# Performance work log

Hardware: AMD Instinct MI355X
Metric: run time of the kernel (lower is better)

## Reference

```python
import jax, jax.numpy as jnp
import numpy as np
from jax import lax

Q = 3          # Self-ONN polynomial order
EPS = 1e-5     # InstanceNorm1d eps


def setup_inputs() -> dict:
    key = jax.random.key(0)
    k1, k2, k3 = jax.random.split(key, 3)
    B, Cin, L = 16, 128, 8192
    Cout, K = 128, 3
    x = jax.random.normal(k1, (B, Cin, L), dtype=jnp.float32)
    # Conv1d weight over power-expanded channels: [Cout, Cin*Q, K]
    W = jax.random.normal(k2, (Cout, Cin * Q, K), dtype=jnp.float32) * 0.05
    b = jax.random.normal(k3, (Cout,), dtype=jnp.float32) * 0.05
    return {"x": x, "W": W, "b": b}


def reference(x, W, b):
    x = jnp.repeat(x, 2, axis=-1)
    # Self-ONN power expansion: concat x^1..x^Q along channel dim -> (B, C*Q, 2L)
    powers = jnp.concatenate([x ** (i + 1) for i in range(Q)], axis=1)
    # Conv1d, stride 1, padding 1 (same length)
    out = lax.conv_general_dilated(
        powers, W,
        window_strides=(1,),
        padding=[(1, 1)],
        dimension_numbers=("NCH", "OIH", "NCH"),
    ) + b[None, :, None]
    # InstanceNorm1d (affine=False): normalize over length per (batch, channel)
    mean = jnp.mean(out, axis=-1, keepdims=True)
    var = jnp.var(out, axis=-1, keepdims=True)
    out = (out - mean) * lax.rsqrt(var + EPS)
    # Tanh activation (self.relu is nn.Tanh()); dropout=False -> no-op
    return jnp.tanh(out)
```

## Files before the change

kernel.cpp:

```cpp
#include <hip/hip_runtime.h>
#include <hip/hip_fp16.h>
#include <math.h>

#define BATCH 16
#define CIN   128
#define LIN   8192
#define COUT  128
#define LOUT  16384
#define KEXP  768
#define NT    128
#define NTILES (LIN/NT)
#define PCOLS 130
#define PCPAD 136
#define PSZ   (PCOLS*PCPAD)

typedef _Float16 f16x8 __attribute__((ext_vector_type(8)));
typedef float    f32x4 __attribute__((ext_vector_type(4)));

__global__ void prep_weights(const float* __restrict__ W,
                             _Float16* __restrict__ WE,
                             _Float16* __restrict__ WO) {
  int idx = blockIdx.x * 256 + threadIdx.x;
  int co = idx / KEXP;
  int k  = idx % KEXP;
  int sh = (k >= 384) ? 1 : 0;
  int cq = k - 384 * sh;
  const float* w = W + ((size_t)co * 384 + cq) * 3;
  float we, wo;
  if (sh == 0) { we = w[0];        wo = w[0] + w[1]; }
  else         { we = w[1] + w[2]; wo = w[2];        }
  int q  = cq >> 7;
  int c  = cq & 127;
  int ks = q * 8 + sh * 4 + (c >> 5);
  int kk = c & 31, quad = kk >> 3, j = kk & 7;
  int mtile = co >> 4, l15 = co & 15;
  size_t off = ((size_t)((mtile * 24 + ks) * 64) + quad * 16 + l15) * 8 + j;
  WE[off] = (_Float16)we;
  WO[off] = (_Float16)wo;
}


#define BUILD_PLANE(POW, P) do {                                           \
  _Pragma("unroll")                                                        \
  for (int slot = 0; slot < 5; ++slot) {                                   \
    if (slot < 4 || tail) {                                                \
      f16x8 w;                                                             \
      _Pragma("unroll")                                                    \
      for (int j = 0; j < 8; ++j) {                                        \
        float v = xv[slot][j];                                             \
        float pv = ((POW) == 1) ? v : (((POW) == 2) ? v * v : v * (v * v));\
        w[j] = (_Float16)pv;                                               \
      }                                                                    \
      *(f16x8*)((P) + woff[slot]) = w;                                     \
    }                                                                      \
  }                                                                        \
} while (0)

#define AFLOAD(DST, KS) do {                                               \
  _Pragma("unroll")                                                        \
  for (int fm = 0; fm < 4; ++fm) {                                         \
    int mt = wm * 4 + fm;                                                  \
    DST[fm] = *(const f16x8*)(Wsel + ((size_t)((mt * 24 + (KS)) * 64) + lane) * 8); \
  }                                                                        \
} while (0)

#define BFLOAD(DST, CUR, S) do {                                           \
  _Pragma("unroll")                                                        \
  for (int fn = 0; fn < 4; ++fn) {                                         \
    int colB = wn * 64 + fn * 16 + l15 + (((S) >> 2) + isO);               \
    DST[fn] = *(const f16x8*)((CUR) + colB * PCPAD + ((S) & 3) * 32 + kl); \
  }                                                                        \
} while (0)

__launch_bounds__(512, 2)
__global__ void conv_gemm(const float* __restrict__ x,
                          const _Float16* __restrict__ WE,
                          const _Float16* __restrict__ WO,
                          float* __restrict__ out,
                          float* __restrict__ stats) {
  extern __shared__ char smem[];
  float*    sstats = (float*)smem;
  _Float16* planes = (_Float16*)(smem + 1024);

  const int tile = blockIdx.x;
  const int b    = blockIdx.y;
  const int i0   = tile * NT;
  const int t    = threadIdx.x;
  const int lane = t & 63;
  const int wave = t >> 6;
  const int p    = wave >> 1;
  const int isO  = wave & 1;
  const int wm   = p >> 1, wn = p & 1;
  const int l15  = lane & 15, quad = lane >> 4;
  const int kl   = quad * 8;

  if (t < 128) { sstats[2 * t] = 0.f; sstats[2 * t + 1] = 0.f; }

  const float* xb = x + (size_t)b * CIN * LIN;
  const _Float16* Wsel = isO ? WO : WE;

  float xv[5][8];
  int   woff[5];
  const bool tail = (t < PCOLS * 16 - 2048);
#pragma unroll
  for (int slot = 0; slot < 5; ++slot) {
    const bool tval = (slot < 4) || tail;
    int task = t + 512 * slot;
    int g    = task / PCOLS;
    if (!tval) g = 0;
    int col  = task - g * PCOLS;
    int gi   = i0 - 1 + col;
    woff[slot] = col * PCPAD + g * 8;
    const bool ok = tval && gi >= 0 && gi < LIN;
    const float* px = xb + (size_t)g * 8 * LIN + gi;
#pragma unroll
    for (int j = 0; j < 8; ++j) {
      float v = 0.f;
      if (ok) v = px[(size_t)j * LIN];
      xv[slot][j] = v;
    }
  }

  f32x4 acc[4][4];
  const f32x4 zero = {0.f, 0.f, 0.f, 0.f};
#pragma unroll
  for (int fm = 0; fm < 4; ++fm)
#pragma unroll
    for (int fn = 0; fn < 4; ++fn) acc[fm][fn] = zero;

  f16x8 af[3][4], bf[2][4];
  AFLOAD(af[0], 0);
  AFLOAD(af[1], 1);
  BUILD_PLANE(1, planes);
  __syncthreads();

#pragma unroll
  for (int q = 0; q < 3; ++q) {
    _Float16* cur = planes + (size_t)(q & 1) * PSZ;
    BFLOAD(bf[0], cur, 0);
    if (q == 0)      BUILD_PLANE(2, planes + PSZ);
    else if (q == 1) BUILD_PLANE(3, planes);

#pragma unroll
    for (int s = 0; s < 8; ++s) {
      const int ks = q * 8 + s;
      if (ks + 2 < 24) AFLOAD(af[(ks + 2) % 3], ks + 2);
      if (s < 7)       BFLOAD(bf[(s + 1) & 1], cur, s + 1);
      __builtin_amdgcn_s_setprio(1);
#pragma unroll
      for (int fm = 0; fm < 4; ++fm)
#pragma unroll
        for (int fn = 0; fn < 4; ++fn)
          acc[fm][fn] = __builtin_amdgcn_mfma_f32_16x16x32_f16(af[ks % 3][fm], bf[s & 1][fn], acc[fm][fn], 0, 0, 0);
      __builtin_amdgcn_s_setprio(0);
    }
    __syncthreads();
  }

  float* orow_base = out + (size_t)b * COUT * LOUT + isO;
#pragma unroll
  for (int fm = 0; fm < 4; ++fm) {
#pragma unroll
    for (int r = 0; r < 4; ++r) {
      float s1 = 0.f, s2 = 0.f;
#pragma unroll
      for (int fn = 0; fn < 4; ++fn) {
        float v = acc[fm][fn][r];
        s1 += v;
        s2 += v * v;
      }
#pragma unroll
      for (int off = 8; off >= 1; off >>= 1) {
        s1 += __shfl_xor(s1, off, 64);
        s2 += __shfl_xor(s2, off, 64);
      }
      int co = wm * 64 + fm * 16 + quad * 4 + r;
      if (l15 == 0) {
        atomicAdd(&sstats[2 * co], s1);
        atomicAdd(&sstats[2 * co + 1], s2);
      }
      float* orow = orow_base + (size_t)co * LOUT;
#pragma unroll
      for (int fn = 0; fn < 4; ++fn) {
        int n = i0 + wn * 64 + fn * 16 + l15;
        orow[2 * n] = acc[fm][fn][r];
      }
    }
  }
  __syncthreads();
  if (t < 128) {
    atomicAdd(&stats[((size_t)b * COUT + t) * 2],     sstats[2 * t]);
    atomicAdd(&stats[((size_t)b * COUT + t) * 2 + 1], sstats[2 * t + 1]);
  }
}

__device__ inline float tanh_fast(float z) {
  float e = __expf(2.f * z);
  return 1.f - 2.f * __builtin_amdgcn_rcpf(e + 1.f);
}

__global__ void norm_tanh(float* __restrict__ out, const float* __restrict__ stats) {
  int row = blockIdx.x;
  float s1 = stats[2 * row], s2 = stats[2 * row + 1];
  const float invN = 1.f / (float)LOUT;
  float mean = s1 * invN;
  float var  = fmaxf(s2 * invN - mean * mean, 0.f);
  float inv  = rsqrtf(var + 1e-5f);
  float c0   = -mean * inv;
  float4* p = (float4*)(out + (size_t)row * LOUT);
  for (int i = threadIdx.x; i < LOUT / 4; i += 256) {
    float4 v = p[i];
    v.x = tanh_fast(fmaf(v.x, inv, c0));
    v.y = tanh_fast(fmaf(v.y, inv, c0));
    v.z = tanh_fast(fmaf(v.z, inv, c0));
    v.w = tanh_fast(fmaf(v.w, inv, c0));
    p[i] = v;
  }
}

extern "C" void kernel_launch(void* const* d_in, const int* in_sizes, int n_in,
                              void* d_out, int out_size, void* d_ws, size_t ws_size,
                              hipStream_t stream) {
  const float* x = (const float*)d_in[0];
  const float* W = (const float*)d_in[1];
  float* out = (float*)d_out;

  float*    stats = (float*)d_ws;
  _Float16* WE    = (_Float16*)((char*)d_ws + 16384);
  _Float16* WO    = WE + (size_t)COUT * KEXP;

  hipMemsetAsync(d_ws, 0, 16384, stream);
  prep_weights<<<dim3((COUT * KEXP) / 256), dim3(256), 0, stream>>>(W, WE, WO);

  size_t shmem = 1024 + (size_t)PSZ * 2 * 2;
  hipFuncSetAttribute(reinterpret_cast<const void*>(conv_gemm),
                      hipFuncAttributeMaxDynamicSharedMemorySize, (int)shmem);
  conv_gemm<<<dim3(NTILES, BATCH), dim3(512), shmem, stream>>>(x, WE, WO, out, stats);

  norm_tanh<<<dim3(BATCH * COUT), dim3(256), 0, stream>>>(out, stats);
}
```

Measured before the change: 276.5 us.

## Persistent conv GEMM with prefetched x tiles, fp16 powers and fp16 intermediate

The conv GEMM becomes persistent: 256 blocks each process four (batch, tile) work items, and the next item's x columns are gathered while the current item's MFMAs run. The x^2 and x^3 planes are now built in fp16 from the x plane in LDS instead of from fp32 registers. Stats go straight to global atomics without the per-block LDS reduction. When the workspace is large enough, the pre-normalisation output is stored as fp16 and read back by norm_tanh, halving that round trip, at the cost of precision before normalisation.

```diff
diff --git a/kernel.cpp b/kernel.cpp
--- a/kernel.cpp
+++ b/kernel.cpp
@@ -13,6 +13,7 @@
 #define PCOLS 130
 #define PCPAD 136
 #define PSZ   (PCOLS*PCPAD)
+#define NITEMS 4
 
 typedef _Float16 f16x8 __attribute__((ext_vector_type(8)));
 typedef float    f32x4 __attribute__((ext_vector_type(4)));
@@ -40,87 +41,107 @@
 }
 
 
-#define BUILD_PLANE(POW, P) do {                                           \
+#define AFLOAD(DST, KS) do {                                               \
+  _Pragma("unroll")                                                        \
+  for (int fm = 0; fm < 4; ++fm) {                                         \
+    int mt = wm * 4 + fm;                                                  \
+    DST[fm] = *(const f16x8*)(Wsel + ((size_t)((mt * 24 + (KS)) * 64) + lane) * 8); \
+  }                                                                        \
+} while (0)
+
+#define BFLOAD(DST, P, S) do {                                             \
+  const _Float16* pb = (P) + (((S) & 3) * 32) + kl;                        \
+  const int shft = (((S) >> 2) + isO);                                     \
+  _Pragma("unroll")                                                        \
+  for (int fn = 0; fn < 4; ++fn) {                                         \
+    int colB = wn * 64 + fn * 16 + l15 + shft;                             \
+    DST[fn] = *(const f16x8*)(pb + colB * PCPAD);                          \
+  }                                                                        \
+} while (0)
+
+#define BUILD_SQ(SRC, DST) do {                                            \
+  _Pragma("unroll")                                                        \
+  for (int slot = 0; slot < 5; ++slot) {                                   \
+    if (slot < 4 || tail) {                                                \
+      f16x8 v = *(f16x8*)((SRC) + woffv[slot]);                            \
+      *(f16x8*)((DST) + woffv[slot]) = v * v;                              \
+    }                                                                      \
+  }                                                                        \
+} while (0)
+
+#define BUILD_CU(P1P, P2P) do {                                            \
+  _Pragma("unroll")                                                        \
+  for (int slot = 0; slot < 5; ++slot) {                                   \
+    if (slot < 4 || tail) {                                                \
+      f16x8 v1 = *(f16x8*)((P1P) + woffv[slot]);                           \
+      f16x8 v2 = *(f16x8*)((P2P) + woffv[slot]);                           \
+      *(f16x8*)((P1P) + woffv[slot]) = v1 * v2;                            \
+    }                                                                      \
+  }                                                                        \
+} while (0)
+
+#define XGATHER(WI) do {                                                   \
+  const float* xbn = x + (size_t)((WI) >> 6) * CIN * LIN;                  \
+  const int i0n = ((WI) & 63) * NT;                                        \
+  _Pragma("unroll")                                                        \
+  for (int slot = 0; slot < 5; ++slot) {                                   \
+    const bool tval = (slot < 4) || tail;                                  \
+    int gi = i0n - 1 + colv[slot];                                         \
+    const bool ok = tval && gi >= 0 && gi < LIN;                           \
+    const float* px = xbn + (size_t)gv[slot] * 8 * LIN + gi;               \
+    _Pragma("unroll")                                                      \
+    for (int j = 0; j < 8; ++j) xn[slot][j] = ok ? px[(size_t)j * LIN] : 0.f; \
+  }                                                                        \
+} while (0)
+
+#define XWRITE(DST) do {                                                   \
   _Pragma("unroll")                                                        \
   for (int slot = 0; slot < 5; ++slot) {                                   \
     if (slot < 4 || tail) {                                                \
       f16x8 w;                                                             \
       _Pragma("unroll")                                                    \
-      for (int j = 0; j < 8; ++j) {                                        \
-        float v = xv[slot][j];                                             \
-        float pv = ((POW) == 1) ? v : (((POW) == 2) ? v * v : v * (v * v));\
-        w[j] = (_Float16)pv;                                               \
-      }                                                                    \
-      *(f16x8*)((P) + woff[slot]) = w;                                     \
+      for (int j = 0; j < 8; ++j) w[j] = (_Float16)xn[slot][j];            \
+      *(f16x8*)((DST) + woffv[slot]) = w;                                  \
     }                                                                      \
   }                                                                        \
 } while (0)
 
-#define AFLOAD(DST, KS) do {                                               \
-  _Pragma("unroll")                                                        \
-  for (int fm = 0; fm < 4; ++fm) {                                         \
-    int mt = wm * 4 + fm;                                                  \
-    DST[fm] = *(const f16x8*)(Wsel + ((size_t)((mt * 24 + (KS)) * 64) + lane) * 8); \
-  }                                                                        \
-} while (0)
-
-#define BFLOAD(DST, CUR, S) do {                                           \
-  _Pragma("unroll")                                                        \
-  for (int fn = 0; fn < 4; ++fn) {                                         \
-    int colB = wn * 64 + fn * 16 + l15 + (((S) >> 2) + isO);               \
-    DST[fn] = *(const f16x8*)((CUR) + colB * PCPAD + ((S) & 3) * 32 + kl); \
-  }                                                                        \
-} while (0)
-
+template<int F16OUT>
 __launch_bounds__(512, 2)
 __global__ void conv_gemm(const float* __restrict__ x,
                           const _Float16* __restrict__ WE,
                           const _Float16* __restrict__ WO,
                           float* __restrict__ out,
+                          _Float16* __restrict__ out16,
                           float* __restrict__ stats) {
   extern __shared__ char smem[];
-  float*    sstats = (float*)smem;
-  _Float16* planes = (_Float16*)(smem + 1024);
-
-  const int tile = blockIdx.x;
-  const int b    = blockIdx.y;
-  const int i0   = tile * NT;
+  _Float16* planes = (_Float16*)smem;
+
+  const int bid  = blockIdx.x;
   const int t    = threadIdx.x;
   const int lane = t & 63;
   const int wave = t >> 6;
-  const int p    = wave >> 1;
   const int isO  = wave & 1;
-  const int wm   = p >> 1, wn = p & 1;
+  const int wn   = (wave >> 1) & 1;
+  const int wm   = wave >> 2;
   const int l15  = lane & 15, quad = lane >> 4;
   const int kl   = quad * 8;
 
-  if (t < 128) { sstats[2 * t] = 0.f; sstats[2 * t + 1] = 0.f; }
-
-  const float* xb = x + (size_t)b * CIN * LIN;
   const _Float16* Wsel = isO ? WO : WE;
 
-  float xv[5][8];
-  int   woff[5];
   const bool tail = (t < PCOLS * 16 - 2048);
+  int colv[5], gv[5], woffv[5];
 #pragma unroll
   for (int slot = 0; slot < 5; ++slot) {
-    const bool tval = (slot < 4) || tail;
     int task = t + 512 * slot;
     int g    = task / PCOLS;
-    if (!tval) g = 0;
     int col  = task - g * PCOLS;
-    int gi   = i0 - 1 + col;
-    woff[slot] = col * PCPAD + g * 8;
-    const bool ok = tval && gi >= 0 && gi < LIN;
-    const float* px = xb + (size_t)g * 8 * LIN + gi;
-#pragma unroll
-    for (int j = 0; j < 8; ++j) {
-      float v = 0.f;
-      if (ok) v = px[(size_t)j * LIN];
-      xv[slot][j] = v;
-    }
+    colv[slot]  = col;
+    gv[slot]    = g;
+    woffv[slot] = col * PCPAD + g * 8;
   }
 
+  float xn[5][8];
   f32x4 acc[4][4];
   const f32x4 zero = {0.f, 0.f, 0.f, 0.f};
 #pragma unroll
@@ -131,66 +152,90 @@
   f16x8 af[3][4], bf[2][4];
   AFLOAD(af[0], 0);
   AFLOAD(af[1], 1);
-  BUILD_PLANE(1, planes);
+
+  XGATHER(bid);
+  XWRITE(planes);
   __syncthreads();
-
-#pragma unroll
-  for (int q = 0; q < 3; ++q) {
-    _Float16* cur = planes + (size_t)(q & 1) * PSZ;
-    BFLOAD(bf[0], cur, 0);
-    if (q == 0)      BUILD_PLANE(2, planes + PSZ);
-    else if (q == 1) BUILD_PLANE(3, planes);
-
-#pragma unroll
-    for (int s = 0; s < 8; ++s) {
-      const int ks = q * 8 + s;
-      if (ks + 2 < 24) AFLOAD(af[(ks + 2) % 3], ks + 2);
-      if (s < 7)       BFLOAD(bf[(s + 1) & 1], cur, s + 1);
-      __builtin_amdgcn_s_setprio(1);
-#pragma unroll
-      for (int fm = 0; fm < 4; ++fm)
-#pragma unroll
-        for (int fn = 0; fn < 4; ++fn)
-          acc[fm][fn] = __builtin_amdgcn_mfma_f32_16x16x32_f16(af[ks % 3][fm], bf[s & 1][fn], acc[fm][fn], 0, 0, 0);
-      __builtin_amdgcn_s_setprio(0);
+  BFLOAD(bf[0], planes, 0);
+
+  for (int item = 0; item < NITEMS; ++item) {
+    _Float16* cur = planes + (size_t)(item & 1) * PSZ;
+    _Float16* oth = planes + (size_t)((item & 1) ^ 1) * PSZ;
+    const int wiN = bid + 256 * (item + 1);
+    const bool more = (item < NITEMS - 1);
+
+#pragma unroll
+    for (int q = 0; q < 3; ++q) {
+      const _Float16* pq = (q == 1) ? oth : cur;
+#pragma unroll
+      for (int s = 0; s < 8; ++s) {
+        const int ks = q * 8 + s;
+        AFLOAD(af[(ks + 2) % 3], (ks + 2) % 24);
+        if (s < 7) BFLOAD(bf[(s + 1) & 1], pq, s + 1);
+        if (q == 0 && s == 0) BUILD_SQ(cur, oth);
+        if (q == 1 && s == 0) BUILD_CU(cur, oth);
+        if (q == 1 && s == 4) { if (more) XGATHER(wiN); }
+        if (q == 2 && s == 4) { if (more) XWRITE(oth); }
+        __builtin_amdgcn_s_setprio(1);
+#pragma unroll
+        for (int fm = 0; fm < 4; ++fm)
+#pragma unroll
+          for (int fn = 0; fn < 4; ++fn)
+            acc[fm][fn] = __builtin_amdgcn_mfma_f32_16x16x32_f16(af[ks % 3][fm], bf[s & 1][fn], acc[fm][fn], 0, 0, 0);
+        __builtin_amdgcn_s_setprio(0);
+      }
+      __syncthreads();
+      if (q == 0)      BFLOAD(bf[0], oth, 0);
+      else if (q == 1) BFLOAD(bf[0], cur, 0);
+      else if (more)   BFLOAD(bf[0], oth, 0);
     }
-    __syncthreads();
-  }
-
-  float* orow_base = out + (size_t)b * COUT * LOUT + isO;
-#pragma unroll
-  for (int fm = 0; fm < 4; ++fm) {
-#pragma unroll
-    for (int r = 0; r < 4; ++r) {
-      float s1 = 0.f, s2 = 0.f;
-#pragma unroll
-      for (int fn = 0; fn < 4; ++fn) {
-        float v = acc[fm][fn][r];
-        s1 += v;
-        s2 += v * v;
-      }
-#pragma unroll
-      for (int off = 8; off >= 1; off >>= 1) {
-        s1 += __shfl_xor(s1, off, 64);
-        s2 += __shfl_xor(s2, off, 64);
-      }
-      int co = wm * 64 + fm * 16 + quad * 4 + r;
-      if (l15 == 0) {
-        atomicAdd(&sstats[2 * co], s1);
-        atomicAdd(&sstats[2 * co + 1], s2);
-      }
-      float* orow = orow_base + (size_t)co * LOUT;
-#pragma unroll
-      for (int fn = 0; fn < 4; ++fn) {
-        int n = i0 + wn * 64 + fn * 16 + l15;
-        orow[2 * n] = acc[fm][fn][r];
+
+    const int wi = bid + 256 * item;
+    const int b  = wi >> 6;
+    const int i0 = (wi & 63) * NT;
+#pragma unroll
+    for (int fm = 0; fm < 4; ++fm) {
+#pragma unroll
+      for (int r = 0; r < 4; ++r) {
+        float s1 = 0.f, s2 = 0.f;
+#pragma unroll
+        for (int fn = 0; fn < 4; ++fn) {
+          float v = acc[fm][fn][r];
+          s1 += v;
+          s2 += v * v;
+        }
+#pragma unroll
+        for (int off = 8; off >= 1; off >>= 1) {
+          s1 += __shfl_xor(s1, off, 64);
+          s2 += __shfl_xor(s2, off, 64);
+        }
+        int co = wm * 64 + fm * 16 + quad * 4 + r;
+        if (l15 == 0) {
+          atomicAdd(&stats[((size_t)b * COUT + co) * 2],     s1);
+          atomicAdd(&stats[((size_t)b * COUT + co) * 2 + 1], s2);
+        }
+        if (F16OUT) {
+          _Float16* orow = out16 + ((size_t)b * COUT + co) * LOUT + isO;
+#pragma unroll
+          for (int fn = 0; fn < 4; ++fn) {
+            int n = i0 + wn * 64 + fn * 16 + l15;
+            orow[2 * n] = (_Float16)acc[fm][fn][r];
+          }
+        } else {
+          float* orow = out + ((size_t)b * COUT + co) * LOUT + isO;
+#pragma unroll
+          for (int fn = 0; fn < 4; ++fn) {
+            int n = i0 + wn * 64 + fn * 16 + l15;
+            orow[2 * n] = acc[fm][fn][r];
+          }
+        }
+        acc[fm][r < 4 ? 0 : 0][0] = acc[fm][0][0];
       }
     }
-  }
-  __syncthreads();
-  if (t < 128) {
-    atomicAdd(&stats[((size_t)b * COUT + t) * 2],     sstats[2 * t]);
-    atomicAdd(&stats[((size_t)b * COUT + t) * 2 + 1], sstats[2 * t + 1]);
+#pragma unroll
+    for (int fm = 0; fm < 4; ++fm)
+#pragma unroll
+      for (int fn = 0; fn < 4; ++fn) acc[fm][fn] = zero;
   }
 }
 
@@ -199,7 +244,9 @@
   return 1.f - 2.f * __builtin_amdgcn_rcpf(e + 1.f);
 }
 
-__global__ void norm_tanh(float* __restrict__ out, const float* __restrict__ stats) {
+template<int F16IN>
+__global__ void norm_tanh(float* __restrict__ out, const _Float16* __restrict__ in16,
+                          const float* __restrict__ stats) {
   int row = blockIdx.x;
   float s1 = stats[2 * row], s2 = stats[2 * row + 1];
   const float invN = 1.f / (float)LOUT;
@@ -207,14 +254,42 @@
   float var  = fmaxf(s2 * invN - mean * mean, 0.f);
   float inv  = rsqrtf(var + 1e-5f);
   float c0   = -mean * inv;
-  float4* p = (float4*)(out + (size_t)row * LOUT);
-  for (int i = threadIdx.x; i < LOUT / 4; i += 256) {
-    float4 v = p[i];
-    v.x = tanh_fast(fmaf(v.x, inv, c0));
-    v.y = tanh_fast(fmaf(v.y, inv, c0));
-    v.z = tanh_fast(fmaf(v.z, inv, c0));
-    v.w = tanh_fast(fmaf(v.w, inv, c0));
-    p[i] = v;
+  if (F16IN) {
+    const f16x8* prow = (const f16x8*)(in16 + (size_t)row * LOUT);
+    f32x4* orow = (f32x4*)(out + (size_t)row * LOUT);
+#pragma unroll
+    for (int u = 0; u < 8; ++u) {
+      int c = threadIdx.x + 256 * u;
+      f16x8 h = prow[c];
+      f32x4 a, bq;
+      a[0] = tanh_fast(fmaf((float)h[0], inv, c0));
+      a[1] = tanh_fast(fmaf((float)h[1], inv, c0));
+      a[2] = tanh_fast(fmaf((float)h[2], inv, c0));
+      a[3] = tanh_fast(fmaf((float)h[3], inv, c0));
+      bq[0] = tanh_fast(fmaf((float)h[4], inv, c0));
+      bq[1] = tanh_fast(fmaf((float)h[5], inv, c0));
+      bq[2] = tanh_fast(fmaf((float)h[6], inv, c0));
+      bq[3] = tanh_fast(fmaf((float)h[7], inv, c0));
+      orow[2 * c]     = a;
+      orow[2 * c + 1] = bq;
+    }
+  } else {
+    float4* p = (float4*)(out + (size_t)row * LOUT);
+#pragma unroll
+    for (int mi = 0; mi < 4; ++mi) {
+      float4 v[4];
+#pragma unroll
+      for (int u = 0; u < 4; ++u) v[u] = p[threadIdx.x + 256 * (mi * 4 + u)];
+#pragma unroll
+      for (int u = 0; u < 4; ++u) {
+        v[u].x = tanh_fast(fmaf(v[u].x, inv, c0));
+        v[u].y = tanh_fast(fmaf(v[u].y, inv, c0));
+        v[u].z = tanh_fast(fmaf(v[u].z, inv, c0));
+        v[u].w = tanh_fast(fmaf(v[u].w, inv, c0));
+      }
+#pragma unroll
+      for (int u = 0; u < 4; ++u) p[threadIdx.x + 256 * (mi * 4 + u)] = v[u];
+    }
   }
 }
 
@@ -228,14 +303,23 @@
   float*    stats = (float*)d_ws;
   _Float16* WE    = (_Float16*)((char*)d_ws + 16384);
   _Float16* WO    = WE + (size_t)COUT * KEXP;
+  _Float16* O16   = (_Float16*)((char*)d_ws + 409600);
+  const size_t need16 = 409600 + (size_t)BATCH * COUT * LOUT * sizeof(_Float16);
+  const bool f16path = ws_size >= need16;
 
   hipMemsetAsync(d_ws, 0, 16384, stream);
   prep_weights<<<dim3((COUT * KEXP) / 256), dim3(256), 0, stream>>>(W, WE, WO);
 
-  size_t shmem = 1024 + (size_t)PSZ * 2 * 2;
-  hipFuncSetAttribute(reinterpret_cast<const void*>(conv_gemm),
-                      hipFuncAttributeMaxDynamicSharedMemorySize, (int)shmem);
-  conv_gemm<<<dim3(NTILES, BATCH), dim3(512), shmem, stream>>>(x, WE, WO, out, stats);
-
-  norm_tanh<<<dim3(BATCH * COUT), dim3(256), 0, stream>>>(out, stats);
-}
+  size_t shmem = (size_t)PSZ * 2 * 2;
+  if (f16path) {
+    hipFuncSetAttribute(reinterpret_cast<const void*>(&conv_gemm<1>),
+                        hipFuncAttributeMaxDynamicSharedMemorySize, (int)shmem);
+    conv_gemm<1><<<dim3(256), dim3(512), shmem, stream>>>(x, WE, WO, out, O16, stats);
+    norm_tanh<1><<<dim3(BATCH * COUT), dim3(256), 0, stream>>>(out, O16, stats);
+  } else {
+    hipFuncSetAttribute(reinterpret_cast<const void*>(&conv_gemm<0>),
+                        hipFuncAttributeMaxDynamicSharedMemorySize, (int)shmem);
+    conv_gemm<0><<<dim3(256), dim3(512), shmem, stream>>>(x, WE, WO, out, O16, stats);
+    norm_tanh<0><<<dim3(BATCH * COUT), dim3(256), 0, stream>>>(out, O16, stats);
+  }
+}
```

After: 644.6 us. 2.33x slower.
